# Kernel optimization log

Hardware: AMD Instinct MI355X
Metric: run time of the kernel (lower is better)

## Reference

```python
import jax, jax.numpy as jnp
import numpy as np

IN_F = 175
HID = 1024
OUT_F = 175


def setup_inputs() -> dict:
    key = jax.random.key(0)
    ks = jax.random.split(key, 16)
    B, T = 128, 200
    s = 0.02
    w = lambda k, shape: (jax.random.normal(k, shape, jnp.float32) * s)
    return {
        "real_seq": jax.random.normal(ks[0], (B, T, IN_F), jnp.float32),
        "W_ih1": w(ks[1], (4 * HID, IN_F)), "W_hh1": w(ks[2], (4 * HID, HID)),
        "b_ih1": w(ks[3], (4 * HID,)), "b_hh1": w(ks[4], (4 * HID,)),
        "W_ih2": w(ks[5], (4 * HID, HID)), "W_hh2": w(ks[6], (4 * HID, HID)),
        "b_ih2": w(ks[7], (4 * HID,)), "b_hh2": w(ks[8], (4 * HID,)),
        "W_ih3": w(ks[9], (4 * HID, HID)), "W_hh3": w(ks[10], (4 * HID, HID)),
        "b_ih3": w(ks[11], (4 * HID,)), "b_hh3": w(ks[12], (4 * HID,)),
        "W_dec": w(ks[13], (OUT_F, HID)), "b_dec": w(ks[14], (OUT_F,)),
    }


def _condition_mask(seq_len, condition_num=5, groundtruth_num=5):
    gt = np.ones((100, groundtruth_num))
    con = np.zeros((100, condition_num))
    lst = np.concatenate((gt, con), 1).reshape(-1)[:seq_len]
    return jnp.asarray(lst.astype(bool))


def _lstm_cell(x, h, c, Wih, Whh, bih, bhh):
    # PyTorch LSTMCell: gate order i, f, g, o
    gates = x @ Wih.T + h @ Whh.T + bih + bhh
    i, f, g, o = jnp.split(gates, 4, axis=-1)
    c_new = jax.nn.sigmoid(f) * c + jax.nn.sigmoid(i) * jnp.tanh(g)
    h_new = jax.nn.sigmoid(o) * jnp.tanh(c_new)
    return h_new, c_new


def reference(real_seq, W_ih1, W_hh1, b_ih1, b_hh1,
              W_ih2, W_hh2, b_ih2, b_hh2,
              W_ih3, W_hh3, b_ih3, b_hh3,
              W_dec, b_dec):
    B, T, _ = real_seq.shape
    H = W_hh1.shape[1]
    Fo = W_dec.shape[0]
    cond = _condition_mask(T)
    z = jnp.zeros((B, H), real_seq.dtype)
    carry0 = (z, z, z, z, z, z, jnp.zeros((B, Fo), real_seq.dtype))

    def step(carry, xs):
        h0, h1, h2, c0, c1, c2, out_frame = carry
        x_t, use_gt = xs
        in_frame = jnp.where(use_gt, x_t, out_frame)
        nh0, nc0 = _lstm_cell(in_frame, h0, c0, W_ih1, W_hh1, b_ih1, b_hh1)
        # NOTE: source feeds the PREVIOUS h0 / h1 to layers 2 / 3 (faithful)
        nh1, nc1 = _lstm_cell(h0, h1, c1, W_ih2, W_hh2, b_ih2, b_hh2)
        nh2, nc2 = _lstm_cell(h1, h2, c2, W_ih3, W_hh3, b_ih3, b_hh3)
        out = nh2 @ W_dec.T + b_dec
        return (nh0, nh1, nh2, nc0, nc1, nc2, out), out

    _, outs = jax.lax.scan(step, carry0,
                           (jnp.transpose(real_seq, (1, 0, 2)), cond))
    # [T, B, Fo] -> [B, T*Fo] (matches torch.cat along dim 1 per step)
    return jnp.transpose(outs, (1, 0, 2)).reshape(B, T * Fo)
```

## Files before the change

kernel.cpp:

```cpp
#include <hip/hip_runtime.h>

#define B_ 128
#define T_ 200
#define INF_ 175
#define INFP_ 192
#define H_ 1024
#define G4_ 4096
#define OUTF_ 175
#define BH3_ (3 * B_ * H_)
#define NCELL 192
#define NDEC 22
#define NWORK (NCELL + NDEC)
#define NBLK (NWORK + 1)
#define SP 16
#define SACC_S 17

typedef __bf16 bf16x8 __attribute__((ext_vector_type(8)));
typedef float f32x4 __attribute__((ext_vector_type(4)));

__device__ __attribute__((aligned(16))) __bf16 g_Wih1p[G4_ * INFP_];
__device__ __attribute__((aligned(16))) __bf16 g_Whh1[G4_ * H_];
__device__ __attribute__((aligned(16))) __bf16 g_Wih2[G4_ * H_];
__device__ __attribute__((aligned(16))) __bf16 g_Whh2[G4_ * H_];
__device__ __attribute__((aligned(16))) __bf16 g_Wih3[G4_ * H_];
__device__ __attribute__((aligned(16))) __bf16 g_Whh3[G4_ * H_];
__device__ __attribute__((aligned(16))) __bf16 g_Wdec[OUTF_ * H_];
__device__ float g_bsum[3 * G4_];
__device__ float g_bdec[OUTF_];
__device__ __attribute__((aligned(16))) __bf16 g_h[2][BH3_];
__device__ __attribute__((aligned(16))) __bf16 g_infp[B_ * INFP_];
__device__ __attribute__((aligned(16))) __bf16 g_xp[(long)T_ * B_ * INFP_];
__device__ int g_isf32;
__device__ int g_flags[256 * SP];
__device__ int g_dflags[32 * SP];
__device__ int g_gen8[8 * SP];
__device__ int g_iready8[8 * SP];

__device__ __forceinline__ f32x4 mfma_bf16(bf16x8 a, bf16x8 b, f32x4 c) {
    return __builtin_amdgcn_mfma_f32_16x16x32_bf16(a, b, c, 0, 0, 0);
}
__device__ __forceinline__ bf16x8 ld8(const __bf16* p) {
    return *reinterpret_cast<const bf16x8*>(p);
}
__device__ __forceinline__ float sigm(float x) { return 1.f / (1.f + expf(-x)); }
__device__ __forceinline__ float rdf(const void* p, long i, int f32) {
    return f32 ? ((const float*)p)[i] : (float)((const __bf16*)p)[i];
}
__device__ __forceinline__ unsigned short bf2u(__bf16 v) {
    union { __bf16 b; unsigned short u; } c; c.b = v; return c.u;
}

__device__ __forceinline__ void lds_barrier() {
    asm volatile("s_waitcnt lgkmcnt(0)" ::: "memory");
    __builtin_amdgcn_s_barrier();
}

__device__ __forceinline__ void spin_rmw(int* addr, int target, int iters) {
    for (int it = 0; it < iters; ++it) {
        if (__hip_atomic_fetch_max(addr, 0, __ATOMIC_RELAXED, __HIP_MEMORY_SCOPE_AGENT) >= target)
            break;
        __builtin_amdgcn_s_sleep(1);
    }
    (void)__hip_atomic_load(addr, __ATOMIC_ACQUIRE, __HIP_MEMORY_SCOPE_AGENT);
}

__global__ void detect_k(const unsigned int* __restrict__ xw) {
    __shared__ int cnt;
    if (threadIdx.x == 0) cnt = 0;
    __syncthreads();
    unsigned int w = xw[threadIdx.x];
    int e = (w >> 7) & 0xFF;
    if (e >= 140) atomicAdd(&cnt, 1);
    __syncthreads();
    if (threadIdx.x == 0) g_isf32 = (cnt >= 16) ? 1 : 0;
}

__global__ void prep_k(const void* Wih1, const void* Whh1, const void* Wih2,
                       const void* Whh2, const void* Wih3, const void* Whh3,
                       const void* Wdec, const void* bih1, const void* bhh1,
                       const void* bih2, const void* bhh2, const void* bih3,
                       const void* bhh3, const void* bdec, const void* xseq) {
    const int f = g_isf32;
    const int idx = blockIdx.x * 256 + threadIdx.x;
    const int stride = gridDim.x * 256;
    if (idx < 256 * SP) g_flags[idx] = 0;
    if (idx < 32 * SP) g_dflags[idx] = 0;
    if (idx < 8 * SP) { g_gen8[idx] = 0; g_iready8[idx] = 0; }
    for (int i = idx; i < G4_ * INFP_; i += stride) {
        int n = i / INFP_, k = i - n * INFP_;
        g_Wih1p[i] = (k < INF_) ? (__bf16)rdf(Wih1, (long)n * INF_ + k, f) : (__bf16)0.f;
    }
    for (int i = idx; i < G4_ * H_; i += stride) {
        g_Whh1[i] = (__bf16)rdf(Whh1, i, f);
        g_Wih2[i] = (__bf16)rdf(Wih2, i, f);
        g_Whh2[i] = (__bf16)rdf(Whh2, i, f);
        g_Wih3[i] = (__bf16)rdf(Wih3, i, f);
        g_Whh3[i] = (__bf16)rdf(Whh3, i, f);
    }
    for (int i = idx; i < OUTF_ * H_; i += stride) g_Wdec[i] = (__bf16)rdf(Wdec, i, f);
    for (int i = idx; i < G4_; i += stride) {
        g_bsum[i]           = rdf(bih1, i, f) + rdf(bhh1, i, f);
        g_bsum[G4_ + i]     = rdf(bih2, i, f) + rdf(bhh2, i, f);
        g_bsum[2 * G4_ + i] = rdf(bih3, i, f) + rdf(bhh3, i, f);
    }
    for (int i = idx; i < OUTF_; i += stride) g_bdec[i] = rdf(bdec, i, f);
    for (int i = idx; i < 2 * BH3_; i += stride) (&g_h[0][0])[i] = (__bf16)0.f;
    for (int i = idx; i < B_ * INFP_; i += stride) g_infp[i] = (__bf16)0.f;
    const long total = (long)T_ * B_ * INFP_;
    for (long i = idx; i < total; i += stride) {
        int k = (int)(i % INFP_);
        long bt = i / INFP_;
        int b = (int)(bt % B_);
        int t = (int)(bt / B_);
        g_xp[((long)t * B_ + b) * INFP_ + k] =
            (k < INF_) ? (__bf16)rdf(xseq, (long)b * (T_ * INF_) + (long)t * INF_ + k, f)
                       : (__bf16)0.f;
    }
}

__device__ __forceinline__ void gridbar_w(int bid, int grp, int target) {
    __syncthreads();
    if (threadIdx.x == 0) {
        __threadfence();
        __hip_atomic_fetch_max(&g_flags[bid * SP], target, __ATOMIC_RELAXED, __HIP_MEMORY_SCOPE_AGENT);
        spin_rmw(&g_gen8[grp * SP], target, 4000);
    }
    __syncthreads();
}

__global__ __launch_bounds__(512, 1) void persist_k(const void* __restrict__ xseq,
                                                    void* __restrict__ dout) {
    __shared__ char s_tile[2][2][16384];
    __shared__ float s_acc[B_ * 4 * SACC_S];
    __shared__ float s_c[B_ * 16];
    __shared__ int s_nf, s_nd;
    const int bid = blockIdx.x;
    const int grp = bid & 7;
    const int tid = threadIdx.x;
    const int lane = tid & 63;
    const int wid = tid >> 6;
    const int rlo = lane & 15, khi = lane >> 4;
    const int f32o = g_isf32;
    const int r7l = rlo & 7;
    const int sw0 = (khi ^ r7l) * 16;
    const int sw1 = ((khi + 4) ^ r7l) * 16;

    if (bid < NCELL) {
        const int L = bid >> 6;
        const int hc0 = (bid & 63) << 4;
        const int op = wid >> 2;
        const int g = wid & 3;
        const float* bs = g_bsum + L * G4_;
        const int XOFF = (L == 0) ? 13 : 0;

        const __bf16* Bm; int K;
        if (op == 0) {
            if (L == 0) { Bm = g_Wih1p; K = INFP_; }
            else        { Bm = (L == 1) ? g_Wih2 : g_Wih3; K = H_; }
        } else {
            Bm = (L == 0) ? g_Whh1 : (L == 1) ? g_Whh2 : g_Whh3; K = H_;
        }
        const __bf16* wp = Bm + (long)(g * H_ + hc0 + rlo) * K + khi * 8;
        bf16x8 wreg[32];
        if (K == INFP_) {
#pragma unroll
            for (int c = 0; c < 6; ++c) wreg[c] = ld8(wp + c * 32);
        } else {
#pragma unroll
            for (int c = 0; c < 32; ++c) wreg[c] = ld8(wp + c * 32);
        }

        const int strow = tid >> 2, stq = tid & 3, str7 = strow & 7;
        auto ldchunk = [&](const __bf16* src, int sA, int k0, bf16x8& v0, bf16x8& v1) {
            const __bf16* pr = src + (long)strow * sA + k0 + stq * 8;
            v0 = ld8(pr);
            v1 = ld8(pr + 32);
        };
        auto wrchunk = [&](char* tile, bf16x8 v0, bf16x8 v1) {
            char* pb = tile + strow * 128;
            *(bf16x8*)(pb + ((stq ^ str7) * 16)) = v0;
            *(bf16x8*)(pb + (((stq + 4) ^ str7) * 16)) = v1;
        };

        for (int i = tid; i < B_ * 16; i += 512) s_c[i] = 0.f;
        __syncthreads();

        for (int p = 0; p < T_; ++p) {
            const bool gt = ((p % 10) < 5);
            const __bf16* hin = g_h[p & 1];
            const __bf16* Apx; int sAx, nx;
            if (L == 0) {
                Apx = gt ? (g_xp + (long)p * B_ * INFP_) : g_infp;
                sAx = INFP_; nx = 3;
            } else {
                Apx = hin + (L - 1) * B_ * H_; sAx = H_; nx = 16;
            }
            const __bf16* Aph = hin + L * B_ * H_;
            const bool needwait = (L == 0) && !gt;

            bf16x8 rx0, rx1, rh0, rh1;
            ldchunk(Aph, H_, 0, rh0, rh1);
            if (XOFF == 0) ldchunk(Apx, sAx, 0, rx0, rx1);
            wrchunk(&s_tile[0][1][0], rh0, rh1);
            if (XOFF == 0) wrchunk(&s_tile[0][0][0], rx0, rx1);
            ldchunk(Aph, H_, 64, rh0, rh1);
            if (XOFF == 0) ldchunk(Apx, sAx, 64, rx0, rx1);
            lds_barrier();

            f32x4 acc[8] = {};
            int buf = 0;
#pragma unroll
            for (int i = 0; i < 16; ++i) {
                if (i < 15) wrchunk(&s_tile[buf ^ 1][1][0], rh0, rh1);
                {
                    int xj = i + 1 - XOFF;
                    if (xj >= 0 && xj < nx) wrchunk(&s_tile[buf ^ 1][0][0], rx0, rx1);
                }
                if (i == 11 && needwait) {
                    if (tid == 0) spin_rmw(&g_iready8[grp * SP], p, 3000);
                    __syncthreads();
                }
                if (i < 14) ldchunk(Aph, H_, (i + 2) * 64, rh0, rh1);
                {
                    int xj = i + 2 - XOFF;
                    if (xj >= 0 && xj < nx) ldchunk(Apx, sAx, xj * 64, rx0, rx1);
                }
                if (op == 1) {
                    const char* tb = &s_tile[buf][1][0];
#pragma unroll
                    for (int mf = 0; mf < 8; ++mf) {
                        const char* rb = tb + (mf * 16 + rlo) * 128;
                        acc[mf] = mfma_bf16(*(const bf16x8*)(rb + sw0), wreg[2 * i], acc[mf]);
                        acc[mf] = mfma_bf16(*(const bf16x8*)(rb + sw1), wreg[2 * i + 1], acc[mf]);
                    }
                } else {
                    int xj = i - XOFF;
                    if (xj >= 0 && xj < nx) {
                        const char* tb = &s_tile[buf][0][0];
#pragma unroll
                        for (int mf = 0; mf < 8; ++mf) {
                            const char* rb = tb + (mf * 16 + rlo) * 128;
                            acc[mf] = mfma_bf16(*(const bf16x8*)(rb + sw0), wreg[2 * xj], acc[mf]);
                            acc[mf] = mfma_bf16(*(const bf16x8*)(rb + sw1), wreg[2 * xj + 1], acc[mf]);
                        }
                    }
                }
                lds_barrier();
                buf ^= 1;
            }

            if (op == 1) {
#pragma unroll
                for (int mf = 0; mf < 8; ++mf)
#pragma unroll
                    for (int j = 0; j < 4; ++j) {
                        int r = mf * 16 + khi * 4 + j;
                        s_acc[(r * 4 + g) * SACC_S + rlo] = acc[mf][j];
                    }
            }
            __syncthreads();
            if (op == 0) {
#pragma unroll
                for (int mf = 0; mf < 8; ++mf)
#pragma unroll
                    for (int j = 0; j < 4; ++j) {
                        int r = mf * 16 + khi * 4 + j;
                        s_acc[(r * 4 + g) * SACC_S + rlo] += acc[mf][j];
                    }
            }
            __syncthreads();

            {
                const int r = wid * 16 + rlo;
                const int hq = khi;
                f32x4 cv = *(const f32x4*)&s_c[r * 16 + hq * 4];
                unsigned long long hbits;
                unsigned short* hp = (unsigned short*)&hbits;
#pragma unroll
                for (int e = 0; e < 4; ++e) {
                    int col = hc0 + hq * 4 + e;
                    float gi_ = s_acc[(r * 4 + 0) * SACC_S + hq * 4 + e] + bs[0 * H_ + col];
                    float gf_ = s_acc[(r * 4 + 1) * SACC_S + hq * 4 + e] + bs[1 * H_ + col];
                    float gg_ = s_acc[(r * 4 + 2) * SACC_S + hq * 4 + e] + bs[2 * H_ + col];
                    float go_ = s_acc[(r * 4 + 3) * SACC_S + hq * 4 + e] + bs[3 * H_ + col];
                    float cn = sigm(gf_) * cv[e] + sigm(gi_) * tanhf(gg_);
                    cv[e] = cn;
                    hp[e] = bf2u((__bf16)(sigm(go_) * tanhf(cn)));
                }
                *(f32x4*)&s_c[r * 16 + hq * 4] = cv;
                __bf16* hdst = g_h[(p + 1) & 1] + L * B_ * H_ + r * H_ + hc0 + hq * 4;
                *(unsigned long long*)hdst = hbits;
            }
            gridbar_w(bid, grp, p + 1);
        }
    } else if (bid < NWORK) {
        const int db = bid - NCELL;
        const int ntile = db % 11, mh = db / 11;
        const int kk = wid >> 2;
        const int mw = wid & 3;
        const int col = ntile * 16 + rlo;
        const int colc = (col < OUTF_) ? col : (OUTF_ - 1);

        const __bf16* pb = g_Wdec + (long)colc * H_ + khi * 8;
        bf16x8 dw[16];
#pragma unroll
        for (int c = 0; c < 16; ++c) dw[c] = ld8(pb + (kk * 16 + c) * 32);

        const int strow = tid >> 3, stc8 = tid & 7, str7 = strow & 7;
        char* const dt0 = &s_tile[0][0][0];
        char* const dt1 = &s_tile[1][0][0];

        auto decwork = [&](int t, bool winf) {
            const bool gtn = (((t + 1) % 10) < 5);
            const __bf16* h2 = g_h[(t + 1) & 1] + 2 * B_ * H_;
            const __bf16* hrow = h2 + (long)(mh * 64 + strow) * H_ + stc8 * 8;
            bf16x8 rv = ld8(hrow);
            *(bf16x8*)(dt0 + strow * 128 + ((stc8 ^ str7) * 16)) = rv;
            rv = ld8(hrow + 64);
            lds_barrier();
            f32x4 acc = {};
            int b = 0;
#pragma unroll
            for (int i = 0; i < 16; ++i) {
                if (i < 15) *(bf16x8*)((b ? dt0 : dt1) + strow * 128 + ((stc8 ^ str7) * 16)) = rv;
                if (i < 14) rv = ld8(hrow + (i + 2) * 64);
                {
                    const char* rb = (b ? dt1 : dt0) + (mw * 16 + rlo) * 128;
                    bf16x8 a0 = *(const bf16x8*)(rb + sw0);
                    bf16x8 a1 = *(const bf16x8*)(rb + sw1);
                    if (i < 8) {
                        if (kk == 0) {
                            acc = mfma_bf16(a0, dw[2 * i], acc);
                            acc = mfma_bf16(a1, dw[2 * i + 1], acc);
                        }
                    } else {
                        if (kk == 1) {
                            acc = mfma_bf16(a0, dw[2 * i - 16], acc);
                            acc = mfma_bf16(a1, dw[2 * i - 15], acc);
                        }
                    }
                }
                lds_barrier();
                b ^= 1;
            }
            if (kk == 1) {
#pragma unroll
                for (int j = 0; j < 4; ++j)
                    s_acc[(mw * 16 + khi * 4 + j) * SACC_S + rlo] = acc[j];
            }
            __syncthreads();
            if (kk == 0) {
#pragma unroll
                for (int j = 0; j < 4; ++j)
                    acc[j] += s_acc[(mw * 16 + khi * 4 + j) * SACC_S + rlo];
                if (col < OUTF_) {
                    const float bias = g_bdec[col];
#pragma unroll
                    for (int j = 0; j < 4; ++j) {
                        int row = mh * 64 + mw * 16 + khi * 4 + j;
                        float ov = acc[j] + bias;
                        long oidx = (long)row * (T_ * OUTF_) + (long)t * OUTF_ + col;
                        if (f32o) __builtin_nontemporal_store(ov, (float*)dout + oidx);
                        else __builtin_nontemporal_store(bf2u((__bf16)ov), (unsigned short*)dout + oidx);
                        if (winf && !gtn) {
                            ((unsigned short*)g_infp)[row * INFP_ + col] = bf2u((__bf16)ov);
                        }
                    }
                }
            }
            __syncthreads();
            if (tid == 0) {
                __threadfence();
                __hip_atomic_fetch_max(&g_dflags[db * SP], t + 1, __ATOMIC_RELAXED, __HIP_MEMORY_SCOPE_AGENT);
            }
        };

        for (int p = 0; p < T_; ++p) {
            if (p >= 1) decwork(p - 1, true);
            gridbar_w(bid, grp, p + 1);
        }
        decwork(T_ - 1, false);
    } else {
        for (int p = 0; p < T_; ++p) {
            const int tgt = p + 1;
            bool ir_done = false;
            for (int it = 0; it < 2000; ++it) {
                if (tid == 0) { s_nf = 0; s_nd = 0; }
                __syncthreads();
                int bad_f = 0, bad_d = 0;
                if (tid < NWORK)
                    bad_f = (__hip_atomic_fetch_max(&g_flags[tid * SP], 0, __ATOMIC_RELAXED, __HIP_MEMORY_SCOPE_AGENT) < tgt);
                if (!ir_done && tid < NDEC)
                    bad_d = (__hip_atomic_fetch_max(&g_dflags[tid * SP], 0, __ATOMIC_RELAXED, __HIP_MEMORY_SCOPE_AGENT) < p);
                if (bad_f) s_nf = 1;
                if (bad_d) s_nd = 1;
                __syncthreads();
                if (!ir_done && !s_nd) {
                    if (tid < 8)
                        __hip_atomic_fetch_max(&g_iready8[tid * SP], p, __ATOMIC_RELAXED, __HIP_MEMORY_SCOPE_AGENT);
                    ir_done = true;
                }
                if (!s_nf) break;
                __builtin_amdgcn_s_sleep(1);
            }
            if (!ir_done && tid < 8)
                __hip_atomic_fetch_max(&g_iready8[tid * SP], p, __ATOMIC_RELAXED, __HIP_MEMORY_SCOPE_AGENT);
            __syncthreads();
            if (tid < 8)
                __hip_atomic_fetch_max(&g_gen8[tid * SP], tgt, __ATOMIC_RELAXED, __HIP_MEMORY_SCOPE_AGENT);
        }
    }
}

extern "C" void kernel_launch(void* const* d_in, const int* in_sizes, int n_in,
                              void* d_out, int out_size, void* d_ws, size_t ws_size,
                              hipStream_t stream) {
    const void* xseq = d_in[0];
    detect_k<<<1, 256, 0, stream>>>((const unsigned int*)xseq);
    prep_k<<<2048, 256, 0, stream>>>(d_in[1], d_in[2], d_in[5], d_in[6], d_in[9],
                                     d_in[10], d_in[13], d_in[3], d_in[4], d_in[7],
                                     d_in[8], d_in[11], d_in[12], d_in[14], xseq);
    persist_k<<<NBLK, 512, 0, stream>>>(xseq, d_out);
}
```

Baseline: 6.542 ms.

## Double K-chunk width in cell GEMM pipeline to halve LDS barrier count

The cell blocks' K-loop now stages 128-wide K chunks (256-byte swizzled rows) instead of 64-wide chunks, so each step runs 8 iterations with 4 MFMAs per row fragment instead of 16 iterations with 2. Layer 0 input is padded to 256 instead of 192 to fit whole chunks. The aim is fewer LDS barriers and loop overheads per timestep on the serial recurrent path. In exchange it uses double the shared memory, more staging registers, and extra zero-padded MFMA work on layer 0. The h-state and fed-back decoder-output stores also become nontemporal.

Measured after the change: 7.991 ms. 1.22x slower.

```diff
diff --git a/kernel.cpp b/kernel.cpp
--- a/kernel.cpp
+++ b/kernel.cpp
@@ -3,7 +3,7 @@
 #define B_ 128
 #define T_ 200
 #define INF_ 175
-#define INFP_ 192
+#define IN2_ 256
 #define H_ 1024
 #define G4_ 4096
 #define OUTF_ 175
@@ -18,7 +18,7 @@
 typedef __bf16 bf16x8 __attribute__((ext_vector_type(8)));
 typedef float f32x4 __attribute__((ext_vector_type(4)));
 
-__device__ __attribute__((aligned(16))) __bf16 g_Wih1p[G4_ * INFP_];
+__device__ __attribute__((aligned(16))) __bf16 g_Wih1p[G4_ * IN2_];
 __device__ __attribute__((aligned(16))) __bf16 g_Whh1[G4_ * H_];
 __device__ __attribute__((aligned(16))) __bf16 g_Wih2[G4_ * H_];
 __device__ __attribute__((aligned(16))) __bf16 g_Whh2[G4_ * H_];
@@ -28,8 +28,8 @@
 __device__ float g_bsum[3 * G4_];
 __device__ float g_bdec[OUTF_];
 __device__ __attribute__((aligned(16))) __bf16 g_h[2][BH3_];
-__device__ __attribute__((aligned(16))) __bf16 g_infp[B_ * INFP_];
-__device__ __attribute__((aligned(16))) __bf16 g_xp[(long)T_ * B_ * INFP_];
+__device__ __attribute__((aligned(16))) __bf16 g_infp[B_ * IN2_];
+__device__ __attribute__((aligned(16))) __bf16 g_xp[(long)T_ * B_ * IN2_];
 __device__ int g_isf32;
 __device__ int g_flags[256 * SP];
 __device__ int g_dflags[32 * SP];
@@ -86,8 +86,8 @@
     if (idx < 256 * SP) g_flags[idx] = 0;
     if (idx < 32 * SP) g_dflags[idx] = 0;
     if (idx < 8 * SP) { g_gen8[idx] = 0; g_iready8[idx] = 0; }
-    for (int i = idx; i < G4_ * INFP_; i += stride) {
-        int n = i / INFP_, k = i - n * INFP_;
+    for (int i = idx; i < G4_ * IN2_; i += stride) {
+        int n = i / IN2_, k = i - n * IN2_;
         g_Wih1p[i] = (k < INF_) ? (__bf16)rdf(Wih1, (long)n * INF_ + k, f) : (__bf16)0.f;
     }
     for (int i = idx; i < G4_ * H_; i += stride) {
@@ -105,14 +105,14 @@
     }
     for (int i = idx; i < OUTF_; i += stride) g_bdec[i] = rdf(bdec, i, f);
     for (int i = idx; i < 2 * BH3_; i += stride) (&g_h[0][0])[i] = (__bf16)0.f;
-    for (int i = idx; i < B_ * INFP_; i += stride) g_infp[i] = (__bf16)0.f;
-    const long total = (long)T_ * B_ * INFP_;
+    for (int i = idx; i < B_ * IN2_; i += stride) g_infp[i] = (__bf16)0.f;
+    const long total = (long)T_ * B_ * IN2_;
     for (long i = idx; i < total; i += stride) {
-        int k = (int)(i % INFP_);
-        long bt = i / INFP_;
+        int k = (int)(i % IN2_);
+        long bt = i / IN2_;
         int b = (int)(bt % B_);
         int t = (int)(bt / B_);
-        g_xp[((long)t * B_ + b) * INFP_ + k] =
+        g_xp[((long)t * B_ + b) * IN2_ + k] =
             (k < INF_) ? (__bf16)rdf(xseq, (long)b * (T_ * INF_) + (long)t * INF_ + k, f)
                        : (__bf16)0.f;
     }
@@ -130,10 +130,10 @@
 
 __global__ __launch_bounds__(512, 1) void persist_k(const void* __restrict__ xseq,
                                                     void* __restrict__ dout) {
-    __shared__ char s_tile[2][2][16384];
-    __shared__ float s_acc[B_ * 4 * SACC_S];
+    __shared__ __attribute__((aligned(16))) char s_all[2][2][32768];
     __shared__ float s_c[B_ * 16];
     __shared__ int s_nf, s_nd;
+    float* const s_acc = (float*)&s_all[0][0][0];
     const int bid = blockIdx.x;
     const int grp = bid & 7;
     const int tid = threadIdx.x;
@@ -142,8 +142,10 @@
     const int rlo = lane & 15, khi = lane >> 4;
     const int f32o = g_isf32;
     const int r7l = rlo & 7;
-    const int sw0 = (khi ^ r7l) * 16;
-    const int sw1 = ((khi + 4) ^ r7l) * 16;
+    const int sws0 = ((0 * 4 + khi) ^ r7l) * 16;
+    const int sws1 = ((1 * 4 + khi) ^ r7l) * 16;
+    const int sws2 = ((2 * 4 + khi) ^ r7l) * 16;
+    const int sws3 = ((3 * 4 + khi) ^ r7l) * 16;
 
     if (bid < NCELL) {
         const int L = bid >> 6;
@@ -151,35 +153,39 @@
         const int op = wid >> 2;
         const int g = wid & 3;
         const float* bs = g_bsum + L * G4_;
-        const int XOFF = (L == 0) ? 13 : 0;
+        const int XOFF = (L == 0) ? 6 : 0;
 
         const __bf16* Bm; int K;
         if (op == 0) {
-            if (L == 0) { Bm = g_Wih1p; K = INFP_; }
+            if (L == 0) { Bm = g_Wih1p; K = IN2_; }
             else        { Bm = (L == 1) ? g_Wih2 : g_Wih3; K = H_; }
         } else {
             Bm = (L == 0) ? g_Whh1 : (L == 1) ? g_Whh2 : g_Whh3; K = H_;
         }
         const __bf16* wp = Bm + (long)(g * H_ + hc0 + rlo) * K + khi * 8;
         bf16x8 wreg[32];
-        if (K == INFP_) {
-#pragma unroll
-            for (int c = 0; c < 6; ++c) wreg[c] = ld8(wp + c * 32);
+        if (K == IN2_) {
+#pragma unroll
+            for (int c = 0; c < 8; ++c) wreg[c] = ld8(wp + c * 32);
         } else {
 #pragma unroll
             for (int c = 0; c < 32; ++c) wreg[c] = ld8(wp + c * 32);
         }
 
         const int strow = tid >> 2, stq = tid & 3, str7 = strow & 7;
-        auto ldchunk = [&](const __bf16* src, int sA, int k0, bf16x8& v0, bf16x8& v1) {
-            const __bf16* pr = src + (long)strow * sA + k0 + stq * 8;
-            v0 = ld8(pr);
-            v1 = ld8(pr + 32);
+        const int w0 = ((0 * 4 + stq) ^ str7) * 16;
+        const int w1 = ((1 * 4 + stq) ^ str7) * 16;
+        const int w2 = ((2 * 4 + stq) ^ str7) * 16;
+        const int w3 = ((3 * 4 + stq) ^ str7) * 16;
+        auto ldchunk = [&](const __bf16* src, int sA, int c, bf16x8* v) {
+            const __bf16* pr = src + (long)strow * sA + c * 128 + stq * 8;
+            v[0] = ld8(pr);       v[1] = ld8(pr + 32);
+            v[2] = ld8(pr + 64);  v[3] = ld8(pr + 96);
         };
-        auto wrchunk = [&](char* tile, bf16x8 v0, bf16x8 v1) {
-            char* pb = tile + strow * 128;
-            *(bf16x8*)(pb + ((stq ^ str7) * 16)) = v0;
-            *(bf16x8*)(pb + (((stq + 4) ^ str7) * 16)) = v1;
+        auto wrchunk = [&](char* tile, const bf16x8* v) {
+            char* pb = tile + strow * 256;
+            *(bf16x8*)(pb + w0) = v[0]; *(bf16x8*)(pb + w1) = v[1];
+            *(bf16x8*)(pb + w2) = v[2]; *(bf16x8*)(pb + w3) = v[3];
         };
 
         for (int i = tid; i < B_ * 16; i += 512) s_c[i] = 0.f;
@@ -190,58 +196,62 @@
             const __bf16* hin = g_h[p & 1];
             const __bf16* Apx; int sAx, nx;
             if (L == 0) {
-                Apx = gt ? (g_xp + (long)p * B_ * INFP_) : g_infp;
-                sAx = INFP_; nx = 3;
+                Apx = gt ? (g_xp + (long)p * B_ * IN2_) : g_infp;
+                sAx = IN2_; nx = 2;
             } else {
-                Apx = hin + (L - 1) * B_ * H_; sAx = H_; nx = 16;
+                Apx = hin + (L - 1) * B_ * H_; sAx = H_; nx = 8;
             }
             const __bf16* Aph = hin + L * B_ * H_;
             const bool needwait = (L == 0) && !gt;
 
-            bf16x8 rx0, rx1, rh0, rh1;
-            ldchunk(Aph, H_, 0, rh0, rh1);
-            if (XOFF == 0) ldchunk(Apx, sAx, 0, rx0, rx1);
-            wrchunk(&s_tile[0][1][0], rh0, rh1);
-            if (XOFF == 0) wrchunk(&s_tile[0][0][0], rx0, rx1);
-            ldchunk(Aph, H_, 64, rh0, rh1);
-            if (XOFF == 0) ldchunk(Apx, sAx, 64, rx0, rx1);
+            bf16x8 rh[4], rx[4];
+            ldchunk(Aph, H_, 0, rh);
+            if (XOFF == 0) ldchunk(Apx, sAx, 0, rx);
+            wrchunk(&s_all[0][1][0], rh);
+            if (XOFF == 0) wrchunk(&s_all[0][0][0], rx);
+            ldchunk(Aph, H_, 1, rh);
+            if (XOFF == 0 && nx > 1) ldchunk(Apx, sAx, 1, rx);
             lds_barrier();
 
             f32x4 acc[8] = {};
             int buf = 0;
 #pragma unroll
-            for (int i = 0; i < 16; ++i) {
-                if (i < 15) wrchunk(&s_tile[buf ^ 1][1][0], rh0, rh1);
+            for (int i = 0; i < 8; ++i) {
+                if (i < 7) wrchunk(&s_all[buf ^ 1][1][0], rh);
                 {
                     int xj = i + 1 - XOFF;
-                    if (xj >= 0 && xj < nx) wrchunk(&s_tile[buf ^ 1][0][0], rx0, rx1);
-                }
-                if (i == 11 && needwait) {
+                    if (xj >= 0 && xj < nx) wrchunk(&s_all[buf ^ 1][0][0], rx);
+                }
+                if (i == 4 && needwait) {
                     if (tid == 0) spin_rmw(&g_iready8[grp * SP], p, 3000);
                     __syncthreads();
                 }
-                if (i < 14) ldchunk(Aph, H_, (i + 2) * 64, rh0, rh1);
+                if (i < 6) ldchunk(Aph, H_, i + 2, rh);
                 {
-                    int xj = i + 2 - XOFF;
-                    if (xj >= 0 && xj < nx) ldchunk(Apx, sAx, xj * 64, rx0, rx1);
+                    int xj2 = i + 2 - XOFF;
+                    if (xj2 >= 0 && xj2 < nx) ldchunk(Apx, sAx, xj2, rx);
                 }
                 if (op == 1) {
-                    const char* tb = &s_tile[buf][1][0];
+                    const char* tb = &s_all[buf][1][0];
 #pragma unroll
                     for (int mf = 0; mf < 8; ++mf) {
-                        const char* rb = tb + (mf * 16 + rlo) * 128;
-                        acc[mf] = mfma_bf16(*(const bf16x8*)(rb + sw0), wreg[2 * i], acc[mf]);
-                        acc[mf] = mfma_bf16(*(const bf16x8*)(rb + sw1), wreg[2 * i + 1], acc[mf]);
+                        const char* rb = tb + (mf * 16 + rlo) * 256;
+                        acc[mf] = mfma_bf16(*(const bf16x8*)(rb + sws0), wreg[i * 4 + 0], acc[mf]);
+                        acc[mf] = mfma_bf16(*(const bf16x8*)(rb + sws1), wreg[i * 4 + 1], acc[mf]);
+                        acc[mf] = mfma_bf16(*(const bf16x8*)(rb + sws2), wreg[i * 4 + 2], acc[mf]);
+                        acc[mf] = mfma_bf16(*(const bf16x8*)(rb + sws3), wreg[i * 4 + 3], acc[mf]);
                     }
                 } else {
                     int xj = i - XOFF;
                     if (xj >= 0 && xj < nx) {
-                        const char* tb = &s_tile[buf][0][0];
+                        const char* tb = &s_all[buf][0][0];
 #pragma unroll
                         for (int mf = 0; mf < 8; ++mf) {
-                            const char* rb = tb + (mf * 16 + rlo) * 128;
-                            acc[mf] = mfma_bf16(*(const bf16x8*)(rb + sw0), wreg[2 * xj], acc[mf]);
-                            acc[mf] = mfma_bf16(*(const bf16x8*)(rb + sw1), wreg[2 * xj + 1], acc[mf]);
+                            const char* rb = tb + (mf * 16 + rlo) * 256;
+                            acc[mf] = mfma_bf16(*(const bf16x8*)(rb + sws0), wreg[xj * 4 + 0], acc[mf]);
+                            acc[mf] = mfma_bf16(*(const bf16x8*)(rb + sws1), wreg[xj * 4 + 1], acc[mf]);
+                            acc[mf] = mfma_bf16(*(const bf16x8*)(rb + sws2), wreg[xj * 4 + 2], acc[mf]);
+                            acc[mf] = mfma_bf16(*(const bf16x8*)(rb + sws3), wreg[xj * 4 + 3], acc[mf]);
                         }
                     }
                 }
@@ -289,7 +299,7 @@
                 }
                 *(f32x4*)&s_c[r * 16 + hq * 4] = cv;
                 __bf16* hdst = g_h[(p + 1) & 1] + L * B_ * H_ + r * H_ + hc0 + hq * 4;
-                *(unsigned long long*)hdst = hbits;
+                __builtin_nontemporal_store(hbits, (unsigned long long*)hdst);
             }
             gridbar_w(bid, grp, p + 1);
         }
@@ -300,6 +310,8 @@
         const int mw = wid & 3;
         const int col = ntile * 16 + rlo;
         const int colc = (col < OUTF_) ? col : (OUTF_ - 1);
+        const int dsw0 = (khi ^ r7l) * 16;
+        const int dsw1 = ((khi + 4) ^ r7l) * 16;
 
         const __bf16* pb = g_Wdec + (long)colc * H_ + khi * 8;
         bf16x8 dw[16];
@@ -307,8 +319,9 @@
         for (int c = 0; c < 16; ++c) dw[c] = ld8(pb + (kk * 16 + c) * 32);
 
         const int strow = tid >> 3, stc8 = tid & 7, str7 = strow & 7;
-        char* const dt0 = &s_tile[0][0][0];
-        char* const dt1 = &s_tile[1][0][0];
+        char* const dt0 = &s_all[0][0][0];
+        char* const dt1 = &s_all[0][0][0] + 16384;
+        float* const s_accD = (float*)(&s_all[0][0][0] + 65536);
 
         auto decwork = [&](int t, bool winf) {
             const bool gtn = (((t + 1) % 10) < 5);
@@ -326,8 +339,8 @@
                 if (i < 14) rv = ld8(hrow + (i + 2) * 64);
                 {
                     const char* rb = (b ? dt1 : dt0) + (mw * 16 + rlo) * 128;
-                    bf16x8 a0 = *(const bf16x8*)(rb + sw0);
-                    bf16x8 a1 = *(const bf16x8*)(rb + sw1);
+                    bf16x8 a0 = *(const bf16x8*)(rb + dsw0);
+                    bf16x8 a1 = *(const bf16x8*)(rb + dsw1);
                     if (i < 8) {
                         if (kk == 0) {
                             acc = mfma_bf16(a0, dw[2 * i], acc);
@@ -346,13 +359,13 @@
             if (kk == 1) {
 #pragma unroll
                 for (int j = 0; j < 4; ++j)
-                    s_acc[(mw * 16 + khi * 4 + j) * SACC_S + rlo] = acc[j];
+                    s_accD[(mw * 16 + khi * 4 + j) * SACC_S + rlo] = acc[j];
             }
             __syncthreads();
             if (kk == 0) {
 #pragma unroll
                 for (int j = 0; j < 4; ++j)
-                    acc[j] += s_acc[(mw * 16 + khi * 4 + j) * SACC_S + rlo];
+                    acc[j] += s_accD[(mw * 16 + khi * 4 + j) * SACC_S + rlo];
                 if (col < OUTF_) {
                     const float bias = g_bdec[col];
 #pragma unroll
@@ -363,7 +376,8 @@
                         if (f32o) __builtin_nontemporal_store(ov, (float*)dout + oidx);
                         else __builtin_nontemporal_store(bf2u((__bf16)ov), (unsigned short*)dout + oidx);
                         if (winf && !gtn) {
-                            ((unsigned short*)g_infp)[row * INFP_ + col] = bf2u((__bf16)ov);
+                            __builtin_nontemporal_store(bf2u((__bf16)ov),
+                                (unsigned short*)g_infp + row * IN2_ + col);
                         }
                     }
                 }
```
